# Performance work log

Hardware: AMD Instinct MI355X
Metric: run time of the kernel (lower is better)

Reference implementation:

```python
import jax, jax.numpy as jnp
import numpy as np

N, E, D, H = 40000, 640000, 128, 8
DH = D // H  # out_feats per head
EPS = 1e-5


def _layernorm(x, g, b):
    mu = jnp.mean(x, axis=-1, keepdims=True)
    var = jnp.mean(jnp.square(x - mu), axis=-1, keepdims=True)
    return (x - mu) * jax.lax.rsqrt(var + EPS) * g + b


def setup_inputs() -> dict:
    key = jax.random.key(0)
    ks = jax.random.split(key, 12)
    s = 0.02
    return {
        "feat": jax.random.normal(ks[0], (N, D), dtype=jnp.float32),
        "src": jax.random.randint(ks[1], (E,), 0, N, dtype=jnp.int32),
        "dst": jax.random.randint(ks[2], (E,), 0, N, dtype=jnp.int32),
        "Wq": jax.random.normal(ks[3], (D, D), dtype=jnp.float32) * s,
        "Wk": jax.random.normal(ks[4], (D, D), dtype=jnp.float32) * s,
        "Wv": jax.random.normal(ks[5], (D, D), dtype=jnp.float32) * s,
        "ln1_g": jnp.ones((D,), jnp.float32),
        "ln1_b": jnp.zeros((D,), jnp.float32),
        "ln2_g": jnp.ones((D,), jnp.float32),
        "ln2_b": jnp.zeros((D,), jnp.float32),
        "W1": jax.random.normal(ks[6], (D, 4 * D), dtype=jnp.float32) * s,
        "b1": jnp.zeros((4 * D,), jnp.float32),
        "prelu_w": jnp.full((4 * D,), 0.25, jnp.float32),
        "W2": jax.random.normal(ks[7], (4 * D, D), dtype=jnp.float32) * s,
        "b2": jnp.zeros((D,), jnp.float32),
    }


def reference(feat, src, dst, Wq, Wk, Wv, ln1_g, ln1_b, ln2_g, ln2_b,
              W1, b1, prelu_w, W2, b2):
    n = feat.shape[0]
    feat_c = jax.lax.stop_gradient(feat)  # .clone().detach()
    q = (feat @ Wq).reshape(n, H, DH)
    k = (feat_c @ Wk).reshape(n, H, DH)
    v = (feat_c @ Wv).reshape(n, H, DH)

    # u_dot_v: per-edge, per-head dot product of k at src and q at dst
    scores = jnp.einsum('ehd,ehd->eh', k[src], q[dst]) / np.float32(np.sqrt(DH * H))

    # edge_softmax: softmax over incoming edges of each destination node
    smax = jax.ops.segment_max(scores, dst, num_segments=n)  # [N,H]
    sexp = jnp.exp(scores - smax[dst])
    ssum = jax.ops.segment_sum(sexp, dst, num_segments=n)
    a = sexp / ssum[dst]  # [E,H]  (attn_drop is eval no-op)

    # u_mul_e + sum: weighted scatter-aggregate of v[src] into dst
    msgs = v[src] * a[:, :, None]  # [E,H,DH]
    ft2 = jax.ops.segment_sum(msgs, dst, num_segments=n).reshape(n, D)

    rst = _layernorm(ft2 + feat, ln1_g, ln1_b)
    h = rst @ W1 + b1
    h = jnp.where(h >= 0, h, prelu_w * h)  # PReLU, per-channel
    ffn = h @ W2 + b2  # ffn_drop is eval no-op
    return _layernorm(rst + ffn, ln2_g, ln2_b)
```

## Files before the change

kernel.cpp:

```cpp
#include <hip/hip_runtime.h>
#include <hip/hip_bf16.h>
#include <math.h>

#define DIM 128
#define NHEAD 8
#define DHEAD 16
#define HID 512
#define LN_EPS 1e-5f
#define SCORE_SCALE 0.08838834764831845f

typedef __bf16 bf16x8 __attribute__((ext_vector_type(8)));
typedef float f32x4 __attribute__((ext_vector_type(4)));

__device__ inline float bf2f(unsigned int bits16) {
    return __uint_as_float(bits16 << 16);
}
__device__ inline unsigned short f2bf(float f) {
    unsigned int u = __float_as_uint(f);
    unsigned int r = u + 0x7fff + ((u >> 16) & 1);
    return (unsigned short)(r >> 16);
}

__device__ inline void gload_lds16(const void* g, void* l) {
    __builtin_amdgcn_global_load_lds(
        (const __attribute__((address_space(1))) unsigned int*)g,
        (__attribute__((address_space(3))) unsigned int*)l, 16, 0, 0);
}

__global__ __launch_bounds__(256) void prep_kernel(
        int* counts, int Nn,
        const float* __restrict__ feat, unsigned short* __restrict__ featb,
        const float* __restrict__ Wq, const float* __restrict__ Wk, const float* __restrict__ Wv,
        unsigned short* __restrict__ Wqkvt,
        const float* __restrict__ W1, unsigned short* __restrict__ W1t,
        const float* __restrict__ W2, unsigned short* __restrict__ W2t,
        int zb, int fb) {
    int blk = blockIdx.x, t = threadIdx.x;
    if (blk < zb) {
        int i = blk * 1024 + t * 4;
        if (i < Nn) *(int4*)(counts + i) = make_int4(0, 0, 0, 0);
    } else if (blk < fb) {
        int i = (blk - zb) * 256 + t;
        if (i < Nn * 32) {
            float4 v = *(const float4*)(feat + (size_t)i * 4);
            ushort4 o;
            o.x = f2bf(v.x); o.y = f2bf(v.y); o.z = f2bf(v.z); o.w = f2bf(v.w);
            *(ushort4*)(featb + (size_t)i * 4) = o;
        }
    } else {
        int b2_ = blk - fb;
        if (b2_ < 192) {
            int sec = b2_ >> 6;
            const float* W = sec == 0 ? Wq : (sec == 1 ? Wk : Wv);
            int o = (b2_ & 63) * 256 + t;
            int oc = o >> 7, orow = o & 127;
            Wqkvt[sec * 16384 + o] = f2bf(W[(size_t)orow * 128 + oc]);
        } else if (b2_ < 448) {
            int o = (b2_ - 192) * 256 + t;
            int oc = o >> 7, orow = o & 127;
            W1t[o] = f2bf(W1[(size_t)orow * 512 + oc]);
        } else {
            int o = (b2_ - 448) * 256 + t;
            int oc = o >> 9, orow = o & 511;
            W2t[o] = f2bf(W2[(size_t)orow * 128 + oc]);
        }
    }
}


__global__ void count_kernel(const int* __restrict__ dst, int* counts, int E) {
    int e = blockIdx.x * blockDim.x + threadIdx.x;
    if (e < E) atomicAdd(&counts[dst[e]], 1);
}

__global__ __launch_bounds__(256) void scanA_kernel(const int* __restrict__ counts, int* bsum, int Nn) {
    int blk = blockIdx.x, t = threadIdx.x;
    int i = blk * 1024 + t * 4;
    int s = 0;
    if (i < Nn) { int4 x = *(const int4*)(counts + i); s = x.x + x.y + x.z + x.w; }
#pragma unroll
    for (int off = 1; off < 64; off <<= 1) s += __shfl_xor(s, off, 64);
    __shared__ int wt[4];
    if ((t & 63) == 0) wt[t >> 6] = s;
    __syncthreads();
    if (t == 0) bsum[blk] = wt[0] + wt[1] + wt[2] + wt[3];
}

__global__ void scanB_kernel(const int* __restrict__ bsum, int* bbase, int* offsets, int nch, int Nn) {
    int t = threadIdx.x;
    int v = (t < nch) ? bsum[t] : 0;
    int s = v;
#pragma unroll
    for (int off = 1; off < 64; off <<= 1) {
        int u = __shfl_up(s, off, 64);
        if (t >= off) s += u;
    }
    if (t < nch) bbase[t] = s - v;
    if (t == 63) offsets[Nn] = s;
}

__global__ __launch_bounds__(256) void scanC_kernel(int* counts, const int* __restrict__ bbase,
                                                    int* offsets, int Nn) {
    int blk = blockIdx.x, t = threadIdx.x, lane = t & 63, wv = t >> 6;
    int i = blk * 1024 + t * 4;
    int4 x = make_int4(0, 0, 0, 0);
    if (i < Nn) x = *(const int4*)(counts + i);
    int ts = x.x + x.y + x.z + x.w;
    int s = ts;
#pragma unroll
    for (int off = 1; off < 64; off <<= 1) {
        int u = __shfl_up(s, off, 64);
        if (lane >= off) s += u;
    }
    __shared__ int wt[4];
    if (lane == 63) wt[wv] = s;
    __syncthreads();
    int woff = 0;
    for (int wi = 0; wi < wv; ++wi) woff += wt[wi];
    int excl = bbase[blk] + woff + (s - ts);
    if (i < Nn) {
        int o0 = excl, o1 = o0 + x.x, o2 = o1 + x.y, o3 = o2 + x.z;
        *(int4*)(offsets + i) = make_int4(o0, o1, o2, o3);
        *(int4*)(counts + i) = make_int4(o0, o1, o2, o3);
    }
}

__global__ void fill_kernel(const int* __restrict__ dst, const int* __restrict__ src,
                            int* cursor, int* srcs, int E) {
    int e = blockIdx.x * blockDim.x + threadIdx.x;
    if (e < E) {
        int pos = atomicAdd(&cursor[dst[e]], 1);
        srcs[pos] = src[e];
    }
}

__global__ __launch_bounds__(256) void qkv_gemm(
        const unsigned short* __restrict__ A, const unsigned short* __restrict__ Bt,
        unsigned short* __restrict__ qb, unsigned short* __restrict__ kv) {
    __shared__ unsigned short As[128 * 32];
    __shared__ unsigned short Bs[128 * 32];
    int t = threadIdx.x;
    int wave = t >> 6, lane = t & 63;
    int wr = wave >> 1, wc = wave & 1;
    int lrow = lane & 15, kq = lane >> 4;
    int m0 = blockIdx.y * 128;
    int region = blockIdx.x;
    int n0 = region * 128;
    int srow = t >> 2, scol8 = (t & 3) * 8;

    f32x4 acc[4][4] = {};
    for (int k0 = 0; k0 < 128; k0 += 32) {
        gload_lds16(A + (size_t)(m0 + srow) * 128 + k0 + scol8,      As + t * 8);
        gload_lds16(A + (size_t)(m0 + 64 + srow) * 128 + k0 + scol8, As + 2048 + t * 8);
        gload_lds16(Bt + (size_t)(n0 + srow) * 128 + k0 + scol8,      Bs + t * 8);
        gload_lds16(Bt + (size_t)(n0 + 64 + srow) * 128 + k0 + scol8, Bs + 2048 + t * 8);
        __syncthreads();
        bf16x8 af[4], bfr[4];
#pragma unroll
        for (int mi = 0; mi < 4; ++mi)
            af[mi] = *(const bf16x8*)(&As[(wr * 64 + mi * 16 + lrow) * 32 + kq * 8]);
#pragma unroll
        for (int ni = 0; ni < 4; ++ni)
            bfr[ni] = *(const bf16x8*)(&Bs[(wc * 64 + ni * 16 + lrow) * 32 + kq * 8]);
#pragma unroll
        for (int mi = 0; mi < 4; ++mi)
#pragma unroll
            for (int ni = 0; ni < 4; ++ni)
                acc[mi][ni] = __builtin_amdgcn_mfma_f32_16x16x32_bf16(af[mi], bfr[ni], acc[mi][ni], 0, 0, 0);
        __syncthreads();
    }
#pragma unroll
    for (int ni = 0; ni < 4; ++ni) {
        int j = wc * 64 + ni * 16 + lrow;
#pragma unroll
        for (int mi = 0; mi < 4; ++mi) {
#pragma unroll
            for (int r = 0; r < 4; ++r) {
                int row = m0 + wr * 64 + mi * 16 + kq * 4 + r;
                unsigned short h = f2bf(acc[mi][ni][r]);
                if (region == 0)
                    qb[(size_t)row * 128 + j] = h;
                else
                    kv[(size_t)row * 256 + (j >> 1) * 4 + (region == 2 ? 2 : 0) + (j & 1)] = h;
            }
        }
    }
}

__global__ __launch_bounds__(256) void agg_ln1_kernel(
        const unsigned short* __restrict__ qb, const unsigned short* __restrict__ kv,
        const float* __restrict__ feat,
        const int* __restrict__ srcs, const int* __restrict__ offsets,
        const float* __restrict__ g, const float* __restrict__ b,
        float* __restrict__ rstf, unsigned short* __restrict__ rstb, int n) {
    int node = blockIdx.x * 4 + (threadIdx.x >> 6);
    int lane = threadIdx.x & 63;
    if (node >= n) return;

    unsigned int qw = ((const unsigned int*)qb)[(size_t)node * 64 + lane];
    float q0 = bf2f(qw & 0xffffu), q1 = bf2f(qw >> 16);
    const uint2* kvw = (const uint2*)kv;

    int beg = offsets[node], end = offsets[node + 1];
    float m = -INFINITY, l = 0.f, a0 = 0.f, a1 = 0.f;

    int idx = beg;
    for (; idx + 8 <= end; idx += 8) {
        int s[8];
#pragma unroll
        for (int i = 0; i < 8; ++i) s[i] = srcs[idx + i];
        uint2 kvp[8];
#pragma unroll
        for (int i = 0; i < 8; ++i) kvp[i] = kvw[(size_t)s[i] * 64 + lane];
        float sc[8];
#pragma unroll
        for (int i = 0; i < 8; ++i) {
            float p = bf2f(kvp[i].x & 0xffffu) * q0 + bf2f(kvp[i].x >> 16) * q1;
            p += __shfl_xor(p, 1, 8);
            p += __shfl_xor(p, 2, 8);
            p += __shfl_xor(p, 4, 8);
            sc[i] = p * SCORE_SCALE;
        }
        float mn = m;
#pragma unroll
        for (int i = 0; i < 8; ++i) mn = fmaxf(mn, sc[i]);
        float f = __expf(m - mn);
        float wsum = 0.f, d0 = 0.f, d1 = 0.f;
#pragma unroll
        for (int i = 0; i < 8; ++i) {
            float w = __expf(sc[i] - mn);
            wsum += w;
            d0 += w * bf2f(kvp[i].y & 0xffffu);
            d1 += w * bf2f(kvp[i].y >> 16);
        }
        l = l * f + wsum;
        a0 = a0 * f + d0;
        a1 = a1 * f + d1;
        m = mn;
    }
    for (; idx < end; ++idx) {
        int s = srcs[idx];
        uint2 kvp = kvw[(size_t)s * 64 + lane];
        float p = bf2f(kvp.x & 0xffffu) * q0 + bf2f(kvp.x >> 16) * q1;
        p += __shfl_xor(p, 1, 8);
        p += __shfl_xor(p, 2, 8);
        p += __shfl_xor(p, 4, 8);
        float sc = p * SCORE_SCALE;
        float mn = fmaxf(m, sc);
        float f = __expf(m - mn), w = __expf(sc - mn);
        l = l * f + w;
        a0 = a0 * f + w * bf2f(kvp.y & 0xffffu);
        a1 = a1 * f + w * bf2f(kvp.y >> 16);
        m = mn;
    }

    float inv = (l > 0.f) ? 1.f / l : 0.f;
    float2 fv = *(const float2*)(feat + (size_t)node * DIM + 2 * lane);
    float x0 = a0 * inv + fv.x;
    float x1 = a1 * inv + fv.y;

    float s1 = x0 + x1;
    float s2 = x0 * x0 + x1 * x1;
#pragma unroll
    for (int off = 1; off < 64; off <<= 1) {
        s1 += __shfl_xor(s1, off, 64);
        s2 += __shfl_xor(s2, off, 64);
    }
    float mean = s1 * (1.f / DIM);
    float var = s2 * (1.f / DIM) - mean * mean;
    float rinv = rsqrtf(var + LN_EPS);
    float g0 = g[2 * lane], g1 = g[2 * lane + 1];
    float b0 = b[2 * lane], b1 = b[2 * lane + 1];
    float o0 = (x0 - mean) * rinv * g0 + b0;
    float o1 = (x1 - mean) * rinv * g1 + b1;
    *(float2*)(rstf + (size_t)node * DIM + 2 * lane) = make_float2(o0, o1);
    unsigned int packed = (unsigned int)f2bf(o0) | ((unsigned int)f2bf(o1) << 16);
    ((unsigned int*)rstb)[(size_t)node * 64 + lane] = packed;
}

#define FST 136
__global__ __launch_bounds__(256, 2) void ffn_fused_kernel(
        const unsigned short* __restrict__ rstb, const float* __restrict__ rstf,
        const unsigned short* __restrict__ W1t, const float* __restrict__ b1,
        const float* __restrict__ prelu,
        const unsigned short* __restrict__ W2t, const float* __restrict__ b2,
        const float* __restrict__ g, const float* __restrict__ bb,
        float* __restrict__ out, int Nn) {
    __shared__ unsigned short As[128 * FST];
    __shared__ unsigned short Hs[128 * FST];
    __shared__ unsigned short Bs[128 * 32];
    __shared__ float red[128][4];

    int t = threadIdx.x, wave = t >> 6, lane = t & 63;
    int lrow = lane & 15, kq = lane >> 4;
    int wr = wave >> 1, wc = wave & 1;
    int m0 = blockIdx.x * 128;
    int srow = t >> 2, scol8 = (t & 3) * 8;

    {
        int row = t >> 1, half = t & 1;
        const float4* src = (const float4*)(rstb + (size_t)(m0 + row) * 128 + half * 64);
        float4* dst = (float4*)(As + row * FST + half * 64);
#pragma unroll
        for (int i = 0; i < 8; ++i) dst[i] = src[i];
    }
    f32x4 facc[4][4] = {};
    __syncthreads();

    for (int c = 0; c < 4; ++c) {
        f32x4 hacc[4][4] = {};
        for (int k0 = 0; k0 < 128; k0 += 32) {
            gload_lds16(W1t + (size_t)(c * 128 + srow) * 128 + k0 + scol8,      Bs + t * 8);
            gload_lds16(W1t + (size_t)(c * 128 + 64 + srow) * 128 + k0 + scol8, Bs + 2048 + t * 8);
            __syncthreads();
            bf16x8 hf[4], nf[4];
#pragma unroll
            for (int hi = 0; hi < 4; ++hi)
                hf[hi] = *(const bf16x8*)(&Bs[(wr * 64 + hi * 16 + lrow) * 32 + kq * 8]);
#pragma unroll
            for (int nj = 0; nj < 4; ++nj)
                nf[nj] = *(const bf16x8*)(&As[(wc * 64 + nj * 16 + lrow) * FST + k0 + kq * 8]);
#pragma unroll
            for (int hi = 0; hi < 4; ++hi)
#pragma unroll
                for (int nj = 0; nj < 4; ++nj)
                    hacc[hi][nj] = __builtin_amdgcn_mfma_f32_16x16x32_bf16(hf[hi], nf[nj], hacc[hi][nj], 0, 0, 0);
            __syncthreads();
        }
#pragma unroll
        for (int hi = 0; hi < 4; ++hi) {
            int hloc = wr * 64 + hi * 16 + kq * 4;
#pragma unroll
            for (int r = 0; r < 4; ++r) {
                int hg = c * 128 + hloc + r;
                float biv = b1[hg], pwv = prelu[hg];
#pragma unroll
                for (int nj = 0; nj < 4; ++nj) {
                    int node = wc * 64 + nj * 16 + lrow;
                    float v = hacc[hi][nj][r] + biv;
                    v = v >= 0.f ? v : pwv * v;
                    Hs[node * FST + hloc + r] = f2bf(v);
                }
            }
        }
        __syncthreads();
        for (int k0 = 0; k0 < 128; k0 += 32) {
            gload_lds16(W2t + (size_t)srow * 512 + c * 128 + k0 + scol8,        Bs + t * 8);
            gload_lds16(W2t + (size_t)(64 + srow) * 512 + c * 128 + k0 + scol8, Bs + 2048 + t * 8);
            __syncthreads();
            bf16x8 af[4], bf2r[4];
#pragma unroll
            for (int mi = 0; mi < 4; ++mi)
                af[mi] = *(const bf16x8*)(&Hs[(wr * 64 + mi * 16 + lrow) * FST + k0 + kq * 8]);
#pragma unroll
            for (int ni = 0; ni < 4; ++ni)
                bf2r[ni] = *(const bf16x8*)(&Bs[(wc * 64 + ni * 16 + lrow) * 32 + kq * 8]);
#pragma unroll
            for (int mi = 0; mi < 4; ++mi)
#pragma unroll
                for (int ni = 0; ni < 4; ++ni)
                    facc[mi][ni] = __builtin_amdgcn_mfma_f32_16x16x32_bf16(af[mi], bf2r[ni], facc[mi][ni], 0, 0, 0);
            __syncthreads();
        }
    }

    float b2v[4], gv[4], bv[4];
    int cols[4];
#pragma unroll
    for (int ni = 0; ni < 4; ++ni) {
        cols[ni] = wc * 64 + ni * 16 + lrow;
        b2v[ni] = b2[cols[ni]]; gv[ni] = g[cols[ni]]; bv[ni] = bb[cols[ni]];
    }
#pragma unroll
    for (int mi = 0; mi < 4; ++mi) {
#pragma unroll
        for (int r = 0; r < 4; ++r) {
            int rloc = wr * 64 + mi * 16 + kq * 4 + r;
            int row = m0 + rloc;
            float ps = 0.f, pq = 0.f;
#pragma unroll
            for (int ni = 0; ni < 4; ++ni) {
                float v = facc[mi][ni][r] + b2v[ni] + rstf[(size_t)row * 128 + cols[ni]];
                facc[mi][ni][r] = v;
                ps += v; pq += v * v;
            }
#pragma unroll
            for (int off = 1; off < 16; off <<= 1) {
                ps += __shfl_xor(ps, off, 16);
                pq += __shfl_xor(pq, off, 16);
            }
            if (lrow == 0) { red[rloc][wc * 2] = ps; red[rloc][wc * 2 + 1] = pq; }
        }
    }
    __syncthreads();
#pragma unroll
    for (int mi = 0; mi < 4; ++mi) {
#pragma unroll
        for (int r = 0; r < 4; ++r) {
            int rloc = wr * 64 + mi * 16 + kq * 4 + r;
            int row = m0 + rloc;
            float s1 = red[rloc][0] + red[rloc][2];
            float s2 = red[rloc][1] + red[rloc][3];
            float mean = s1 * (1.f / DIM);
            float var = s2 * (1.f / DIM) - mean * mean;
            float rs = rsqrtf(var + LN_EPS);
            if (row < Nn) {
#pragma unroll
                for (int ni = 0; ni < 4; ++ni)
                    out[(size_t)row * 128 + cols[ni]] =
                        (facc[mi][ni][r] - mean) * rs * gv[ni] + bv[ni];
            }
        }
    }
}


extern "C" void kernel_launch(void* const* d_in, const int* in_sizes, int n_in,
                              void* d_out, int out_size, void* d_ws, size_t ws_size,
                              hipStream_t stream) {
    const float* feat   = (const float*)d_in[0];
    const int*   src    = (const int*)d_in[1];
    const int*   dst    = (const int*)d_in[2];
    const float* Wq     = (const float*)d_in[3];
    const float* Wk     = (const float*)d_in[4];
    const float* Wv     = (const float*)d_in[5];
    const float* ln1_g  = (const float*)d_in[6];
    const float* ln1_b  = (const float*)d_in[7];
    const float* ln2_g  = (const float*)d_in[8];
    const float* ln2_b  = (const float*)d_in[9];
    const float* W1     = (const float*)d_in[10];
    const float* b1     = (const float*)d_in[11];
    const float* prelu  = (const float*)d_in[12];
    const float* W2     = (const float*)d_in[13];
    const float* b2     = (const float*)d_in[14];
    float* out = (float*)d_out;

    const int Nn = in_sizes[0] / DIM;
    const int E  = in_sizes[1];
    const int MP = (Nn + 127) & ~127;

    char* w = (char*)d_ws;
    unsigned short* qb   = (unsigned short*)w; w += (size_t)MP * DIM * 2;
    unsigned short* kv   = (unsigned short*)w; w += (size_t)MP * 256 * 2;
    float* rstf          = (float*)w;          w += (size_t)MP * DIM * 4;
    unsigned short* rstb = (unsigned short*)w; w += (size_t)MP * DIM * 2;
    unsigned short* featb= (unsigned short*)w; w += (size_t)MP * DIM * 2;
    unsigned short* Wqkvt= (unsigned short*)w; w += 3 * DIM * DIM * 2;
    unsigned short* W1t  = (unsigned short*)w; w += (size_t)HID * DIM * 2;
    unsigned short* W2t  = (unsigned short*)w; w += (size_t)DIM * HID * 2;
    int* counts  = (int*)w;  w += (size_t)Nn * 4;
    int* offsets = (int*)w;  w += (size_t)(Nn + 4) * 4;
    int* bsum    = (int*)w;  w += 64 * 4;
    int* bbase   = (int*)w;  w += 64 * 4;
    int* srcs    = (int*)w;

    const int NCH = (Nn + 1023) / 1024;
    const int zb = NCH;
    const int fb = zb + Nn / 8;

    prep_kernel<<<fb + 192 + 256 + 256, 256, 0, stream>>>(
        counts, Nn, feat, featb, Wq, Wk, Wv, Wqkvt, W1, W1t, W2, W2t, zb, fb);

    count_kernel<<<(E + 255) / 256, 256, 0, stream>>>(dst, counts, E);
    scanA_kernel<<<NCH, 256, 0, stream>>>(counts, bsum, Nn);
    scanB_kernel<<<1, 64, 0, stream>>>(bsum, bbase, offsets, NCH, Nn);
    scanC_kernel<<<NCH, 256, 0, stream>>>(counts, bbase, offsets, Nn);
    fill_kernel<<<(E + 255) / 256, 256, 0, stream>>>(dst, src, counts, srcs, E);

    {
        dim3 grid(3, MP / 128);
        qkv_gemm<<<grid, 256, 0, stream>>>(featb, Wqkvt, qb, kv);
    }

    agg_ln1_kernel<<<(Nn + 3) / 4, 256, 0, stream>>>(qb, kv, feat, srcs, offsets,
                                                     ln1_g, ln1_b, rstf, rstb, Nn);

    ffn_fused_kernel<<<MP / 128, 256, 0, stream>>>(rstb, rstf, W1t, b1, prelu,
                                                   W2t, b2, ln2_g, ln2_b, out, Nn);
}
```

Before: 270.4 us.

## Use fp16 Q/K/V with fdot2, exp2 softmax, merged scan, drop fp32 residual

Q, K and V are now stored as separate fp16 arrays. Q is pre-scaled by the score scale times log2(e), so the aggregation kernel can use packed fdot2 and a native exp2. The GEMM epilogue stages results in LDS and writes coalesced 16-byte stores instead of scattered 2-byte stores. The block-sum scan is folded into scanC, removing one launch. The fp32 rst buffer is dropped and the FFN residual is read from the bf16 copy, which cuts memory traffic but lowers the precision of the residual path.

```diff
diff --git a/kernel.cpp b/kernel.cpp
--- a/kernel.cpp
+++ b/kernel.cpp
@@ -7,10 +7,11 @@
 #define DHEAD 16
 #define HID 512
 #define LN_EPS 1e-5f
-#define SCORE_SCALE 0.08838834764831845f
+#define QSCALE 0.12751879104863297f
 
 typedef __bf16 bf16x8 __attribute__((ext_vector_type(8)));
 typedef float f32x4 __attribute__((ext_vector_type(4)));
+typedef _Float16 f16x2 __attribute__((ext_vector_type(2)));
 
 __device__ inline float bf2f(unsigned int bits16) {
     return __uint_as_float(bits16 << 16);
@@ -19,6 +20,25 @@
     unsigned int u = __float_as_uint(f);
     unsigned int r = u + 0x7fff + ((u >> 16) & 1);
     return (unsigned short)(r >> 16);
+}
+__device__ inline unsigned short f2h(float f) {
+    _Float16 h = (_Float16)f;
+    return __builtin_bit_cast(unsigned short, h);
+}
+__device__ inline float edot2(unsigned int kw, f16x2 q) {
+#if __has_builtin(__builtin_amdgcn_fdot2)
+    return __builtin_amdgcn_fdot2(__builtin_bit_cast(f16x2, kw), q, 0.f, false);
+#else
+    f16x2 k = __builtin_bit_cast(f16x2, kw);
+    return (float)k.x * (float)q.x + (float)k.y * (float)q.y;
+#endif
+}
+__device__ inline float fexp2(float x) {
+#if __has_builtin(__builtin_amdgcn_exp2f)
+    return __builtin_amdgcn_exp2f(x);
+#else
+    return exp2f(x);
+#endif
 }
 
 __device__ inline void gload_lds16(const void* g, void* l) {
@@ -86,22 +106,26 @@
     if (t == 0) bsum[blk] = wt[0] + wt[1] + wt[2] + wt[3];
 }
 
-__global__ void scanB_kernel(const int* __restrict__ bsum, int* bbase, int* offsets, int nch, int Nn) {
-    int t = threadIdx.x;
-    int v = (t < nch) ? bsum[t] : 0;
-    int s = v;
-#pragma unroll
-    for (int off = 1; off < 64; off <<= 1) {
-        int u = __shfl_up(s, off, 64);
-        if (t >= off) s += u;
-    }
-    if (t < nch) bbase[t] = s - v;
-    if (t == 63) offsets[Nn] = s;
-}
-
-__global__ __launch_bounds__(256) void scanC_kernel(int* counts, const int* __restrict__ bbase,
-                                                    int* offsets, int Nn) {
+__global__ __launch_bounds__(256) void scanC_kernel(int* counts, const int* __restrict__ bsum,
+                                                    int* offsets, int Nn, int NCH) {
     int blk = blockIdx.x, t = threadIdx.x, lane = t & 63, wv = t >> 6;
+    __shared__ int wt[4];
+    __shared__ int base_s;
+    if (wv == 0) {
+        int v = (lane < NCH) ? bsum[lane] : 0;
+        int s = v;
+#pragma unroll
+        for (int off = 1; off < 64; off <<= 1) {
+            int u = __shfl_up(s, off, 64);
+            if (lane >= off) s += u;
+        }
+        int basev = (blk > 0) ? __shfl(s, blk - 1, 64) : 0;
+        int tot = __shfl(s, NCH - 1, 64);
+        if (lane == 0) {
+            base_s = basev;
+            if (blk == 0) offsets[Nn] = tot;
+        }
+    }
     int i = blk * 1024 + t * 4;
     int4 x = make_int4(0, 0, 0, 0);
     if (i < Nn) x = *(const int4*)(counts + i);
@@ -112,12 +136,11 @@
         int u = __shfl_up(s, off, 64);
         if (lane >= off) s += u;
     }
-    __shared__ int wt[4];
     if (lane == 63) wt[wv] = s;
     __syncthreads();
     int woff = 0;
     for (int wi = 0; wi < wv; ++wi) woff += wt[wi];
-    int excl = bbase[blk] + woff + (s - ts);
+    int excl = base_s + woff + (s - ts);
     if (i < Nn) {
         int o0 = excl, o1 = o0 + x.x, o2 = o1 + x.y, o3 = o2 + x.z;
         *(int4*)(offsets + i) = make_int4(o0, o1, o2, o3);
@@ -134,11 +157,14 @@
     }
 }
 
+#define QST 136
 __global__ __launch_bounds__(256) void qkv_gemm(
         const unsigned short* __restrict__ A, const unsigned short* __restrict__ Bt,
-        unsigned short* __restrict__ qb, unsigned short* __restrict__ kv) {
-    __shared__ unsigned short As[128 * 32];
-    __shared__ unsigned short Bs[128 * 32];
+        unsigned short* __restrict__ qb, unsigned short* __restrict__ kb,
+        unsigned short* __restrict__ vb) {
+    __shared__ unsigned short smem[128 * QST];
+    unsigned short* As = smem;
+    unsigned short* Bs = smem + 4096;
     int t = threadIdx.x;
     int wave = t >> 6, lane = t & 63;
     int wr = wave >> 1, wc = wave & 1;
@@ -169,37 +195,45 @@
                 acc[mi][ni] = __builtin_amdgcn_mfma_f32_16x16x32_bf16(af[mi], bfr[ni], acc[mi][ni], 0, 0, 0);
         __syncthreads();
     }
+
+    float scale = (region == 0) ? QSCALE : 1.f;
 #pragma unroll
     for (int ni = 0; ni < 4; ++ni) {
-        int j = wc * 64 + ni * 16 + lrow;
+        int col = wc * 64 + ni * 16 + lrow;
 #pragma unroll
         for (int mi = 0; mi < 4; ++mi) {
 #pragma unroll
             for (int r = 0; r < 4; ++r) {
-                int row = m0 + wr * 64 + mi * 16 + kq * 4 + r;
-                unsigned short h = f2bf(acc[mi][ni][r]);
-                if (region == 0)
-                    qb[(size_t)row * 128 + j] = h;
-                else
-                    kv[(size_t)row * 256 + (j >> 1) * 4 + (region == 2 ? 2 : 0) + (j & 1)] = h;
+                int row = wr * 64 + mi * 16 + kq * 4 + r;
+                smem[row * QST + col] = f2h(acc[mi][ni][r] * scale);
             }
         }
     }
+    __syncthreads();
+    unsigned short* outp = (region == 0 ? qb : (region == 1 ? kb : vb)) + (size_t)m0 * 128;
+#pragma unroll
+    for (int i = 0; i < 8; ++i) {
+        int chunk = i * 256 + t;
+        int row = chunk >> 4, c16 = chunk & 15;
+        *(float4*)(outp + (size_t)chunk * 8) = *(const float4*)(smem + row * QST + c16 * 8);
+    }
 }
 
 __global__ __launch_bounds__(256) void agg_ln1_kernel(
-        const unsigned short* __restrict__ qb, const unsigned short* __restrict__ kv,
+        const unsigned short* __restrict__ qb, const unsigned short* __restrict__ kb,
+        const unsigned short* __restrict__ vb,
         const float* __restrict__ feat,
         const int* __restrict__ srcs, const int* __restrict__ offsets,
         const float* __restrict__ g, const float* __restrict__ b,
-        float* __restrict__ rstf, unsigned short* __restrict__ rstb, int n) {
+        unsigned short* __restrict__ rstb, int n) {
     int node = blockIdx.x * 4 + (threadIdx.x >> 6);
     int lane = threadIdx.x & 63;
     if (node >= n) return;
 
-    unsigned int qw = ((const unsigned int*)qb)[(size_t)node * 64 + lane];
-    float q0 = bf2f(qw & 0xffffu), q1 = bf2f(qw >> 16);
-    const uint2* kvw = (const uint2*)kv;
+    const unsigned int* q32 = (const unsigned int*)qb;
+    const unsigned int* k32 = (const unsigned int*)kb;
+    const unsigned int* v32 = (const unsigned int*)vb;
+    f16x2 qp = __builtin_bit_cast(f16x2, q32[(size_t)node * 64 + lane]);
 
     int beg = offsets[node], end = offsets[node + 1];
     float m = -INFINITY, l = 0.f, a0 = 0.f, a1 = 0.f;
@@ -209,29 +243,32 @@
         int s[8];
 #pragma unroll
         for (int i = 0; i < 8; ++i) s[i] = srcs[idx + i];
-        uint2 kvp[8];
-#pragma unroll
-        for (int i = 0; i < 8; ++i) kvp[i] = kvw[(size_t)s[i] * 64 + lane];
+        unsigned int kw[8], vw[8];
+#pragma unroll
+        for (int i = 0; i < 8; ++i) kw[i] = k32[(size_t)s[i] * 64 + lane];
+#pragma unroll
+        for (int i = 0; i < 8; ++i) vw[i] = v32[(size_t)s[i] * 64 + lane];
         float sc[8];
 #pragma unroll
         for (int i = 0; i < 8; ++i) {
-            float p = bf2f(kvp[i].x & 0xffffu) * q0 + bf2f(kvp[i].x >> 16) * q1;
+            float p = edot2(kw[i], qp);
             p += __shfl_xor(p, 1, 8);
             p += __shfl_xor(p, 2, 8);
             p += __shfl_xor(p, 4, 8);
-            sc[i] = p * SCORE_SCALE;
+            sc[i] = p;
         }
         float mn = m;
 #pragma unroll
         for (int i = 0; i < 8; ++i) mn = fmaxf(mn, sc[i]);
-        float f = __expf(m - mn);
+        float f = fexp2(m - mn);
         float wsum = 0.f, d0 = 0.f, d1 = 0.f;
 #pragma unroll
         for (int i = 0; i < 8; ++i) {
-            float w = __expf(sc[i] - mn);
+            float w = fexp2(sc[i] - mn);
+            f16x2 vp = __builtin_bit_cast(f16x2, vw[i]);
             wsum += w;
-            d0 += w * bf2f(kvp[i].y & 0xffffu);
-            d1 += w * bf2f(kvp[i].y >> 16);
+            d0 = fmaf((float)vp.x, w, d0);
+            d1 = fmaf((float)vp.y, w, d1);
         }
         l = l * f + wsum;
         a0 = a0 * f + d0;
@@ -240,17 +277,18 @@
     }
     for (; idx < end; ++idx) {
         int s = srcs[idx];
-        uint2 kvp = kvw[(size_t)s * 64 + lane];
-        float p = bf2f(kvp.x & 0xffffu) * q0 + bf2f(kvp.x >> 16) * q1;
+        unsigned int kw = k32[(size_t)s * 64 + lane];
+        unsigned int vw = v32[(size_t)s * 64 + lane];
+        float p = edot2(kw, qp);
         p += __shfl_xor(p, 1, 8);
         p += __shfl_xor(p, 2, 8);
         p += __shfl_xor(p, 4, 8);
-        float sc = p * SCORE_SCALE;
-        float mn = fmaxf(m, sc);
-        float f = __expf(m - mn), w = __expf(sc - mn);
+        float mn = fmaxf(m, p);
+        float f = fexp2(m - mn), w = fexp2(p - mn);
+        f16x2 vp = __builtin_bit_cast(f16x2, vw);
         l = l * f + w;
-        a0 = a0 * f + w * bf2f(kvp.y & 0xffffu);
-        a1 = a1 * f + w * bf2f(kvp.y >> 16);
+        a0 = a0 * f + w * (float)vp.x;
+        a1 = a1 * f + w * (float)vp.y;
         m = mn;
     }
 
@@ -273,14 +311,13 @@
     float b0 = b[2 * lane], b1 = b[2 * lane + 1];
     float o0 = (x0 - mean) * rinv * g0 + b0;
     float o1 = (x1 - mean) * rinv * g1 + b1;
-    *(float2*)(rstf + (size_t)node * DIM + 2 * lane) = make_float2(o0, o1);
     unsigned int packed = (unsigned int)f2bf(o0) | ((unsigned int)f2bf(o1) << 16);
     ((unsigned int*)rstb)[(size_t)node * 64 + lane] = packed;
 }
 
 #define FST 136
 __global__ __launch_bounds__(256, 2) void ffn_fused_kernel(
-        const unsigned short* __restrict__ rstb, const float* __restrict__ rstf,
+        const unsigned short* __restrict__ rstb,
         const unsigned short* __restrict__ W1t, const float* __restrict__ b1,
         const float* __restrict__ prelu,
         const unsigned short* __restrict__ W2t, const float* __restrict__ b2,
@@ -380,7 +417,8 @@
             float ps = 0.f, pq = 0.f;
 #pragma unroll
             for (int ni = 0; ni < 4; ++ni) {
-                float v = facc[mi][ni][r] + b2v[ni] + rstf[(size_t)row * 128 + cols[ni]];
+                float rsv = bf2f(rstb[(size_t)row * 128 + cols[ni]]);
+                float v = facc[mi][ni][r] + b2v[ni] + rsv;
                 facc[mi][ni][r] = v;
                 ps += v; pq += v * v;
             }
@@ -441,8 +479,8 @@
 
     char* w = (char*)d_ws;
     unsigned short* qb   = (unsigned short*)w; w += (size_t)MP * DIM * 2;
-    unsigned short* kv   = (unsigned short*)w; w += (size_t)MP * 256 * 2;
-    float* rstf          = (float*)w;          w += (size_t)MP * DIM * 4;
+    unsigned short* kb   = (unsigned short*)w; w += (size_t)MP * DIM * 2;
+    unsigned short* vb   = (unsigned short*)w; w += (size_t)MP * DIM * 2;
     unsigned short* rstb = (unsigned short*)w; w += (size_t)MP * DIM * 2;
     unsigned short* featb= (unsigned short*)w; w += (size_t)MP * DIM * 2;
     unsigned short* Wqkvt= (unsigned short*)w; w += 3 * DIM * DIM * 2;
@@ -451,7 +489,6 @@
     int* counts  = (int*)w;  w += (size_t)Nn * 4;
     int* offsets = (int*)w;  w += (size_t)(Nn + 4) * 4;
     int* bsum    = (int*)w;  w += 64 * 4;
-    int* bbase   = (int*)w;  w += 64 * 4;
     int* srcs    = (int*)w;
 
     const int NCH = (Nn + 1023) / 1024;
@@ -463,18 +500,17 @@
 
     count_kernel<<<(E + 255) / 256, 256, 0, stream>>>(dst, counts, E);
     scanA_kernel<<<NCH, 256, 0, stream>>>(counts, bsum, Nn);
-    scanB_kernel<<<1, 64, 0, stream>>>(bsum, bbase, offsets, NCH, Nn);
-    scanC_kernel<<<NCH, 256, 0, stream>>>(counts, bbase, offsets, Nn);
+    scanC_kernel<<<NCH, 256, 0, stream>>>(counts, bsum, offsets, Nn, NCH);
     fill_kernel<<<(E + 255) / 256, 256, 0, stream>>>(dst, src, counts, srcs, E);
 
     {
         dim3 grid(3, MP / 128);
-        qkv_gemm<<<grid, 256, 0, stream>>>(featb, Wqkvt, qb, kv);
-    }
-
-    agg_ln1_kernel<<<(Nn + 3) / 4, 256, 0, stream>>>(qb, kv, feat, srcs, offsets,
-                                                     ln1_g, ln1_b, rstf, rstb, Nn);
-
-    ffn_fused_kernel<<<MP / 128, 256, 0, stream>>>(rstb, rstf, W1t, b1, prelu,
+        qkv_gemm<<<grid, 256, 0, stream>>>(featb, Wqkvt, qb, kb, vb);
+    }
+
+    agg_ln1_kernel<<<(Nn + 3) / 4, 256, 0, stream>>>(qb, kb, vb, feat, srcs, offsets,
+                                                     ln1_g, ln1_b, rstb, Nn);
+
+    ffn_fused_kernel<<<MP / 128, 256, 0, stream>>>(rstb, W1t, b1, prelu,
                                                    W2t, b2, ln2_g, ln2_b, out, Nn);
 }
```

Measured after the change: 262.6 us. 1.03x faster.
